# Optimization experiments

Hardware: AMD Instinct MI355X
Metric: run time of the kernel (lower is better)

Reference implementation:

```python
import jax, jax.numpy as jnp
import numpy as np

# Module-level constants from the original source
VDD = 1.8
Q_BITS_GLOBAL = 3                    # global q_bits fixes Vr regardless of num_of_bits arg
VR = VDD / 2 ** Q_BITS_GLOBAL        # 0.225
VREF = VR
NOISE_SIGMA = 0.01
DELTA = 1e-30

NUM_BITS = 8                         # init arg num_of_bits
NUM_ADCS = 24                        # 2 * p * number_of_samples = 2*3*4
LENGTH = 524288                      # batch of analog samples
M = NUM_BITS * (NUM_BITS + 1) // 2   # required W_tensor leading dim = 36


def setup_inputs() -> dict:
    key = jax.random.key(0)
    k1, k2, k3 = jax.random.split(key, 3)
    x = jax.random.normal(k1, (LENGTH, NUM_ADCS), dtype=jnp.float32)
    W_tensor = jax.random.normal(k2, (M, NUM_ADCS), dtype=jnp.float32)
    noise = jax.random.normal(k3, (M, NUM_ADCS), dtype=jnp.float32)  # per-forward inference noise (std normal)
    return {"x": x, "W_tensor": W_tensor, "noise": noise}


def reference(x, W_tensor, noise):
    # W_noisy = W + randn * noise_sigma**0.5  (noisy_inference=True)
    Wn = W_tensor + noise * (NOISE_SIGMA ** 0.5)   # [M, A]

    B = NUM_BITS
    q_cols = [None] * B
    m = M - 1
    # Bit-serial SAR recurrence: strictly sequential over bits (B=8 static iters)
    for j in reversed(range(B)):
        bit_sum = Wn[m] * VREF                     # [A] broadcast over length
        m -= 1
        for k in range(j + 1, B):
            bit_sum = bit_sum + (q_cols[k] + 1.0) * 0.5 * Wn[m] * VR
            m -= 1
        q_cols[j] = jnp.sign(x - bit_sum + DELTA)  # [L, A]

    Q = jnp.stack(q_cols, axis=-1)                 # [L, A, B]
    bit_weights = VR * (2.0 ** jnp.arange(B, dtype=jnp.float32))  # Vr * 2^b
    q = jnp.sum((Q + 1.0) * 0.5 * bit_weights, axis=-1)           # [L, A]
    return q, Q, Wn
```

## Files before the change

### kernel.cpp

```cpp
#include <hip/hip_runtime.h>


#define L_TOT   524288
#define A_ADC   24
#define M_ROWS  36
#define B_BITS  8
#define BLK     192
#define NBLK    2560
#define NXCD    8
#define N_TOT   (L_TOT * A_ADC)
#define T_STR   (NBLK * BLK)

typedef float f32x4 __attribute__((ext_vector_type(4)));

__device__ __forceinline__ int swz(int c) { return c ^ ((c >> 3) & 7); }

__global__ __launch_bounds__(BLK) void sar_kernel(
    const float* __restrict__ x,
    const float* __restrict__ W,
    const float* __restrict__ nz,
    float* __restrict__ out_q,
    float* __restrict__ out_Q,
    float* __restrict__ out_Wn)
{
    const int bid = blockIdx.x;
    const int sb  = (bid & (NXCD - 1)) * (NBLK / NXCD) + (bid >> 3);

    const int gid = sb * BLK + threadIdx.x;
    const int a = gid % 24;
    const int w = threadIdx.x >> 6;
    const int l = threadIdx.x & 63;

    __shared__ f32x4 stage[BLK / 64][2][128];

    float c[M_ROWS];
#pragma unroll
    for (int r = 0; r < M_ROWS; ++r) {
        float wn = W[r * A_ADC + a] + nz[r * A_ADC + a] * 0.1f;
        c[r] = wn * 0.225f;
    }

    if (gid < M_ROWS * A_ADC) {
        __builtin_nontemporal_store(W[gid] + nz[gid] * 0.1f, &out_Wn[gid]);
    }

    auto sar = [&](float xv) -> unsigned {
        unsigned msk = 0u;
        int m = M_ROWS - 1;
#pragma unroll
        for (int jj = 0; jj < B_BITS; ++jj) {
            const int j = B_BITS - 1 - jj;
            float bs = c[m]; --m;
#pragma unroll
            for (int kk = j + 1; kk < B_BITS; ++kk) {
                bs += ((msk >> kk) & 1u) ? c[m] : 0.0f;
                --m;
            }
            if (xv >= bs) msk |= (1u << j);
        }
        return msk;
    };
    auto qsum = [](unsigned msk) -> float {
        float acc = 0.0f;
#pragma unroll
        for (int j = 0; j < B_BITS; ++j) {
            const float bwj = 0.225f * (float)(1 << j);
            acc += ((msk >> j) & 1u) ? bwj : 0.0f;
        }
        return acc;
    };
    auto qwrite = [&](int i, unsigned msk, int b) {
        f32x4 v0, v1;
#pragma unroll
        for (int j = 0; j < 4; ++j) {
            v0[j] = ((msk >> j) & 1u)       ? 1.0f : -1.0f;
            v1[j] = ((msk >> (j + 4)) & 1u) ? 1.0f : -1.0f;
        }
        const int c0 = 2 * l, c1 = 2 * l + 1;
        stage[w][b][swz(c0)] = v0;
        stage[w][b][swz(c1)] = v1;
        f32x4* Qp = (f32x4*)out_Q + (long long)(i - l) * 2;
        const int r0 = l, r1 = 64 + l;
        __builtin_nontemporal_store(stage[w][b][swz(r0)], &Qp[r0]);
        __builtin_nontemporal_store(stage[w][b][swz(r1)], &Qp[r1]);
    };

    float xv0 = x[gid];
    float xv1 = x[gid + T_STR];

    int i = gid;
    while (i + T_STR < N_TOT) {
        float xn0 = 0.0f, xn1 = 0.0f;
        if (i + 2 * T_STR < N_TOT) xn0 = x[i + 2 * T_STR];
        if (i + 3 * T_STR < N_TOT) xn1 = x[i + 3 * T_STR];

        const unsigned m0 = sar(xv0);
        const unsigned m1 = sar(xv1);

        __builtin_nontemporal_store(qsum(m0), &out_q[i]);
        __builtin_nontemporal_store(qsum(m1), &out_q[i + T_STR]);
        qwrite(i, m0, 0);
        qwrite(i + T_STR, m1, 1);

        xv0 = xn0;
        xv1 = xn1;
        i += 2 * T_STR;
    }
    if (i < N_TOT) {
        const unsigned m0 = sar(xv0);
        __builtin_nontemporal_store(qsum(m0), &out_q[i]);
        qwrite(i, m0, 0);
    }
}

extern "C" void kernel_launch(void* const* d_in, const int* in_sizes, int n_in,
                              void* d_out, int out_size, void* d_ws, size_t ws_size,
                              hipStream_t stream) {
    const float* x  = (const float*)d_in[0];
    const float* W  = (const float*)d_in[1];
    const float* nz = (const float*)d_in[2];
    float* out = (float*)d_out;

    float* out_q  = out;
    float* out_Q  = out + (long long)N_TOT;
    float* out_Wn = out + (long long)N_TOT * 9;

    sar_kernel<<<NBLK, BLK, 0, stream>>>(x, W, nz, out_q, out_Q, out_Wn);
}
```

Measured before the change: 94.65 us.

## Process contiguous 384-element windows per block with block-wide LDS staging

Each block now handles a contiguous window of 384 elements per iteration instead of two grid-strided chunks, with each thread owning fixed ADC column cc so the 36 coefficients match. q and Q results are staged in shared memory, then written out as contiguous vectorized stores: f32x2 for q and four f32x4 stores per thread covering a 12KB Q region. This is meant to make the output writes larger and more contiguous. It adds two __syncthreads per iteration.

Result: slower. 96.84 us (+2.3%).

```diff
diff --git a/kernel.cpp b/kernel.cpp
--- a/kernel.cpp
+++ b/kernel.cpp
@@ -9,11 +9,13 @@
 #define NBLK    2560
 #define NXCD    8
 #define N_TOT   (L_TOT * A_ADC)
-#define T_STR   (NBLK * BLK)
+#define WELEM   384
+#define NWIN    (N_TOT / WELEM)
 
 typedef float f32x4 __attribute__((ext_vector_type(4)));
+typedef float f32x2 __attribute__((ext_vector_type(2)));
 
-__device__ __forceinline__ int swz(int c) { return c ^ ((c >> 3) & 7); }
+__device__ __forceinline__ int swz8(int c) { return c ^ ((c >> 3) & 7); }
 
 __global__ __launch_bounds__(BLK) void sar_kernel(
     const float* __restrict__ x,
@@ -26,20 +28,25 @@
     const int bid = blockIdx.x;
     const int sb  = (bid & (NXCD - 1)) * (NBLK / NXCD) + (bid >> 3);
 
-    const int gid = sb * BLK + threadIdx.x;
-    const int a = gid % 24;
-    const int w = threadIdx.x >> 6;
-    const int l = threadIdx.x & 63;
+    const int tid = threadIdx.x;
+    const int q8  = tid / 24;
+    const int cc  = tid % 24;
+    const int l0  = 48 * q8 + cc;
+    const int l1  = l0 + 24;
+    const int wl  = tid >> 6;
+    const int l   = tid & 63;
 
-    __shared__ f32x4 stage[BLK / 64][2][128];
+    __shared__ f32x4 sQ[WELEM * 2];
+    __shared__ float sq[WELEM];
 
     float c[M_ROWS];
 #pragma unroll
     for (int r = 0; r < M_ROWS; ++r) {
-        float wn = W[r * A_ADC + a] + nz[r * A_ADC + a] * 0.1f;
+        float wn = W[r * A_ADC + cc] + nz[r * A_ADC + cc] * 0.1f;
         c[r] = wn * 0.225f;
     }
 
+    const int gid = sb * BLK + tid;
     if (gid < M_ROWS * A_ADC) {
         __builtin_nontemporal_store(W[gid] + nz[gid] * 0.1f, &out_Wn[gid]);
     }
@@ -69,47 +76,54 @@
         }
         return acc;
     };
-    auto qwrite = [&](int i, unsigned msk, int b) {
-        f32x4 v0, v1;
-#pragma unroll
-        for (int j = 0; j < 4; ++j) {
-            v0[j] = ((msk >> j) & 1u)       ? 1.0f : -1.0f;
-            v1[j] = ((msk >> (j + 4)) & 1u) ? 1.0f : -1.0f;
+
+    int win = sb;
+    float xv0 = x[win * WELEM + l0];
+    float xv1 = x[win * WELEM + l1];
+
+    while (win < NWIN) {
+        const int nwin = win + NBLK;
+        float xn0 = 0.0f, xn1 = 0.0f;
+        if (nwin < NWIN) {
+            xn0 = x[nwin * WELEM + l0];
+            xn1 = x[nwin * WELEM + l1];
         }
-        const int c0 = 2 * l, c1 = 2 * l + 1;
-        stage[w][b][swz(c0)] = v0;
-        stage[w][b][swz(c1)] = v1;
-        f32x4* Qp = (f32x4*)out_Q + (long long)(i - l) * 2;
-        const int r0 = l, r1 = 64 + l;
-        __builtin_nontemporal_store(stage[w][b][swz(r0)], &Qp[r0]);
-        __builtin_nontemporal_store(stage[w][b][swz(r1)], &Qp[r1]);
-    };
-
-    float xv0 = x[gid];
-    float xv1 = x[gid + T_STR];
-
-    int i = gid;
-    while (i + T_STR < N_TOT) {
-        float xn0 = 0.0f, xn1 = 0.0f;
-        if (i + 2 * T_STR < N_TOT) xn0 = x[i + 2 * T_STR];
-        if (i + 3 * T_STR < N_TOT) xn1 = x[i + 3 * T_STR];
 
         const unsigned m0 = sar(xv0);
         const unsigned m1 = sar(xv1);
 
-        __builtin_nontemporal_store(qsum(m0), &out_q[i]);
-        __builtin_nontemporal_store(qsum(m1), &out_q[i + T_STR]);
-        qwrite(i, m0, 0);
-        qwrite(i + T_STR, m1, 1);
+        sq[l0] = qsum(m0);
+        sq[l1] = qsum(m1);
+        f32x4 v0, v1, v2, v3;
+#pragma unroll
+        for (int j = 0; j < 4; ++j) {
+            v0[j] = ((m0 >> j) & 1u)       ? 1.0f : -1.0f;
+            v1[j] = ((m0 >> (j + 4)) & 1u) ? 1.0f : -1.0f;
+            v2[j] = ((m1 >> j) & 1u)       ? 1.0f : -1.0f;
+            v3[j] = ((m1 >> (j + 4)) & 1u) ? 1.0f : -1.0f;
+        }
+        sQ[swz8(2 * l0)]     = v0;
+        sQ[swz8(2 * l0 + 1)] = v1;
+        sQ[swz8(2 * l1)]     = v2;
+        sQ[swz8(2 * l1 + 1)] = v3;
+        __syncthreads();
+
+        {
+            f32x2 qv; qv.x = sq[2 * tid]; qv.y = sq[2 * tid + 1];
+            __builtin_nontemporal_store(
+                qv, (f32x2*)(out_q + (long long)win * WELEM) + tid);
+        }
+        f32x4* Qb = (f32x4*)out_Q + (long long)win * (WELEM * 2);
+#pragma unroll
+        for (int k = 0; k < 4; ++k) {
+            const int ch = wl * 256 + k * 64 + l;
+            __builtin_nontemporal_store(sQ[swz8(ch)], &Qb[ch]);
+        }
+        __syncthreads();
 
         xv0 = xn0;
         xv1 = xn1;
-        i += 2 * T_STR;
-    }
-    if (i < N_TOT) {
-        const unsigned m0 = sar(xv0);
-        __builtin_nontemporal_store(qsum(m0), &out_q[i]);
-        qwrite(i, m0, 0);
+        win = nwin;
     }
 }
 
```
